# Kernel optimization log

Measured on AMD Instinct MI355X. Metric: run time of the kernel, lower is better.

The kernel has to match this reference:

```python
import jax, jax.numpy as jnp
import numpy as np

N_FFT = 2048
HOP = 512
OUT_CH = N_FFT // 2 + 1  # 1025


def _dft_conv_weights():
    # periodic ('fftbins=True') Hann window, win_length == n_fft so no padding
    n = np.arange(N_FFT)
    window = 0.5 - 0.5 * np.cos(2.0 * np.pi * n / N_FFT)
    k = np.arange(OUT_CH)
    ang = 2.0 * np.pi * np.outer(k, n) / N_FFT  # (OUT_CH, N_FFT)
    w_real = (np.cos(ang) * window[None, :]).astype(np.float32)
    w_imag = (-np.sin(ang) * window[None, :]).astype(np.float32)
    return jnp.asarray(w_real), jnp.asarray(w_imag)


def setup_inputs() -> dict:
    key = jax.random.key(0)
    x = jax.random.normal(key, (32, 2, 160000), dtype=jnp.float32)
    W_real, W_imag = _dft_conv_weights()
    return {"x": x, "W_real": W_real, "W_imag": W_imag}


def reference(x, W_real, W_imag):
    # x: (B, C, L). center=True -> reflect pad by n_fft//2 on both sides.
    pad = N_FFT // 2
    x_pad = jnp.pad(x, ((0, 0), (0, 0), (pad, pad)), mode="reflect")
    L = x_pad.shape[-1]
    num_frames = (L - N_FFT) // HOP + 1  # 313
    # frame indices: (T, N_FFT)
    idx = jnp.arange(num_frames)[:, None] * HOP + jnp.arange(N_FFT)[None, :]
    frames = x_pad[..., idx]  # (B, C, T, N_FFT)
    # windowed DFT as matmul (equivalent to the Conv1d with stride=hop)
    real = jnp.einsum("bctn,kn->bctk", frames, W_real)
    imag = jnp.einsum("bctn,kn->bctk", frames, W_imag)
    return real, imag
```

## Files before the change

kernel.cpp:

```cpp
#include <hip/hip_runtime.h>

#define B_     32
#define C_     2
#define L_     160000
#define HOP    512
#define PAD    1024
#define LPAD   162048
#define T_     313
#define BC     64
#define M_     20032
#define KCH    1025
#define OUT_HALF 20532800UL
#define PL     81024
#define KD     1024
#define NKT    32
#define MTP    160
#define NWG    1280
#define LIMW   8336

typedef __attribute__((ext_vector_type(8))) short short8;
typedef __attribute__((ext_vector_type(4))) float f32x4;

static __device__ __forceinline__ short f2bf(float f) {
  union { float f; unsigned u; } v; v.f = f;
  unsigned u = v.u;
  unsigned r = (u + 0x7fffu + ((u >> 16) & 1u)) >> 16;
  return (short)r;
}

__global__ void prep_planes(const float* __restrict__ x,
                            short* __restrict__ pl0, short* __restrict__ pl1) {
  int v = blockIdx.x * 256 + threadIdx.x;
  int bc = v / 10128;
  int r  = v - bc * 10128;
  int p0 = r * 8;
  const float* src = x + (size_t)bc * L_;
  short8 e, o;
  if (r >= 64 && r <= 10000) {
    int j0 = 16 * r - 1024;
    #pragma unroll
    for (int qq = 0; qq < 4; ++qq) {
      float4 f = *(const float4*)(src + j0 + qq * 4);
      e[qq * 2 + 0] = f2bf(f.x); o[qq * 2 + 0] = f2bf(f.y);
      e[qq * 2 + 1] = f2bf(f.z); o[qq * 2 + 1] = f2bf(f.w);
    }
  } else {
    #pragma unroll
    for (int u = 0; u < 16; ++u) {
      int j = 16 * r + u - 1024;
      j = j < 0 ? -j : j;
      j = j >= L_ ? 2 * L_ - 2 - j : j;
      short b = f2bf(src[j]);
      if (u & 1) o[u >> 1] = b; else e[u >> 1] = b;
    }
  }
  *(short8*)&pl0[(size_t)bc * PL + p0] = e;
  *(short8*)&pl1[(size_t)bc * PL + p0] = o;
}

__global__ void prep_wb(short* __restrict__ wb0, short* __restrict__ wb1) {
  int id = blockIdx.x * 256 + threadIdx.x;
  int s   = id >> 17;
  int row = (id >> 7) & 1023;
  int n8  = (id & 127) * 8;
  int kp  = row >> 1, e = row & 1;
  short8 ov;
  #pragma unroll
  for (int u = 0; u < 8; ++u) {
    int n1 = n8 + u;
    float win = 0.5f - 0.5f * cosf((float)(2 * n1 + s) * 3.0679615757712823e-3f);
    float tw;
    if (e == 0)       tw = cosf((float)((n1 * kp) & 1023) * 6.1359231515425649e-3f);
    else if (kp == 0) tw = (n1 & 1) ? -1.0f : 1.0f;
    else              tw = -sinf((float)((n1 * kp) & 1023) * 6.1359231515425649e-3f);
    ov[u] = f2bf(win * tw);
  }
  short* wb = s ? wb1 : wb0;
  *(short8*)&wb[(size_t)row * KD + n8] = ov;
}

#define GLOAD16(g, l) __builtin_amdgcn_global_load_lds(                        \
    (const __attribute__((address_space(1))) void*)(g),                        \
    (__attribute__((address_space(3))) void*)(l), 16, 0, 0)

__global__ __launch_bounds__(512, 4) void stft_gemm(const short* __restrict__ pl0,
                                                    const short* __restrict__ pl1,
                                                    const short* __restrict__ wb0,
                                                    const short* __restrict__ wb1,
                                                    float* __restrict__ out) {
  __shared__ __align__(16) char lds[66688];
  const int tid  = threadIdx.x;
  const int lane = tid & 63;
  const int wid  = tid >> 6;

  const int id = blockIdx.x;
  const int mt = (id & 7) * 20 + (id >> 6);
  const int nt = (id >> 3) & 7;
  const int M0 = mt * 128, N0 = nt * 128;

  const int sw = wid & 1, wn = (wid >> 1) & 1, wm = wid >> 2;

  const int srow  = tid >> 2;
  const int chunk = ((tid & 3) ^ ((tid >> 3) & 3)) * 8;
  const short *a0S, *a1S, *b0S, *b1S;
  {
    int m = M0 + srow; if (m > M_ - 1) m = M_ - 1;
    int bc = m / T_;
    int t  = m - bc * T_;
    size_t base = (size_t)bc * PL + (size_t)t * 256 + chunk;
    a0S = pl0 + base;
    a1S = pl1 + base;
    size_t bb = (size_t)(N0 + srow) * KD + chunk;
    b0S = wb0 + bb;
    b1S = wb1 + bb;
  }
  const int dst = tid * 16;

  const int fr = lane & 15;
  const int xorb = ((lane >> 4) * 16) ^ ((fr & 6) << 3);
  int aOff[4], bOff[4];
  #pragma unroll
  for (int i = 0; i < 4; ++i)
    aOff[i] = sw * 8192 + (wm * 64 + i * 16 + fr) * 64 + xorb;
  #pragma unroll
  for (int j = 0; j < 4; ++j)
    bOff[j] = 16384 + sw * 8192 + (wn * 64 + j * 16 + fr) * 64 + xorb;

  f32x4 acc[4][4];
  #pragma unroll
  for (int i = 0; i < 4; ++i)
    #pragma unroll
    for (int j = 0; j < 4; ++j) acc[i][j] = (f32x4){0.f, 0.f, 0.f, 0.f};

  GLOAD16(a0S, lds + dst);
  GLOAD16(a1S, lds + 8192 + dst);
  GLOAD16(b0S, lds + 16384 + dst);
  GLOAD16(b1S, lds + 24576 + dst);

  for (int kt = 0; kt < NKT; ++kt) {
    char* bufR = lds + (kt & 1) * 32768;
    char* bufW = lds + ((kt + 1) & 1) * 32768;
    const int kos = (kt + 1) * 32;
    const bool st = (kt < NKT - 1);

    if (st) {
      GLOAD16(a0S + kos, bufW + dst);
      GLOAD16(a1S + kos, bufW + 8192 + dst);
      GLOAD16(b0S + kos, bufW + 16384 + dst);
      GLOAD16(b1S + kos, bufW + 24576 + dst);
      asm volatile("s_waitcnt vmcnt(4)" ::: "memory");
    } else {
      asm volatile("s_waitcnt vmcnt(0)" ::: "memory");
    }
    __builtin_amdgcn_s_barrier();

    short8 af[4], bf[4];
    #pragma unroll
    for (int i = 0; i < 4; ++i) af[i] = *(const short8*)(bufR + aOff[i]);
    #pragma unroll
    for (int j = 0; j < 4; ++j) bf[j] = *(const short8*)(bufR + bOff[j]);
    __builtin_amdgcn_s_setprio(1);
    #pragma unroll
    for (int i = 0; i < 4; ++i)
      #pragma unroll
      for (int j = 0; j < 4; ++j)
        acc[i][j] = __builtin_amdgcn_mfma_f32_16x16x32_bf16(af[i], bf[j],
                                                            acc[i][j], 0, 0, 0);
    __builtin_amdgcn_s_setprio(0);
    __builtin_amdgcn_s_barrier();
  }

  float* L = (float*)lds;
  float* outI = out + OUT_HALF;
  const float PIQ = 3.0679615757712823e-3f;
  const int rgrp = (lane >> 4) << 2;

  __syncthreads();

  #pragma unroll
  for (int pass = 0; pass < 2; ++pass) {
    if (sw == 0) {
      #pragma unroll
      for (int j = 0; j < 4; ++j) {
        int c  = wn * 64 + j * 16 + fr;
        int q  = c >> 1;
        bool odd  = c & 1;
        bool spec = (nt == 0) && (c == 1);
        int widx = (odd ? LIMW : 0) + (pass ? (63 - q) : q);
        #pragma unroll
        for (int i = 0; i < 4; ++i) {
          int row = wm * 64 + i * 16 + rgrp;
          #pragma unroll
          for (int r = 0; r < 4; ++r) {
            float v0 = acc[i][j][r];
            float base = pass == 0 ? v0 : (odd ? -v0 : v0);
            if (spec) base = 0.f;
            L[widx + (row + r) * 65] = base;
            if (spec && pass == 0) {
              int gm = M0 + row + r;
              if (gm < M_) out[(size_t)gm * KCH + 512] = v0;
            }
          }
        }
      }
    }
    __syncthreads();
    if (sw == 1) {
      #pragma unroll
      for (int j = 0; j < 4; ++j) {
        int c  = wn * 64 + j * 16 + fr;
        int q  = c >> 1;
        float ang = (float)(nt * 64 + q) * PIQ;
        float tr = cosf(ang), sn = sinf(ang);
        bool odd  = c & 1;
        bool spec = (nt == 0) && (c == 1);
        float sgn = odd ? -sn : sn;
        int widx = (odd ? LIMW : 0) + (pass ? (63 - q) : q);
        #pragma unroll
        for (int i = 0; i < 4; ++i) {
          int row = wm * 64 + i * 16 + rgrp;
          #pragma unroll
          for (int r = 0; r < 4; ++r) {
            float v1 = acc[i][j][r];
            float p1 = __shfl_xor(v1, 1);
            float u  = tr * v1 + sgn * p1;
            if (!spec) {
              float addv = (pass == 0) ? u : (odd ? u : -u);
              int li = widx + (row + r) * 65;
              L[li] += addv;
            } else if (pass == 0) {
              int gm = M0 + row + r;
              if (gm < M_) outI[(size_t)gm * KCH + 512] = -v1;
            }
          }
        }
      }
    }
    __syncthreads();
    {
      int col0 = pass ? (1024 - nt * 64 - 63) : (nt * 64);
      #pragma unroll
      for (int i2 = 0; i2 < 16; ++i2) {
        int row = wid + i2 * 8;
        int gm  = M0 + row;
        if (gm < M_) {
          size_t rb = (size_t)gm * KCH + col0 + lane;
          out [rb] = L[row * 65 + lane];
          outI[rb] = L[LIMW + row * 65 + lane];
        }
      }
    }
    __syncthreads();
  }
}

extern "C" void kernel_launch(void* const* d_in, const int* in_sizes, int n_in,
                              void* d_out, int out_size, void* d_ws, size_t ws_size,
                              hipStream_t stream) {
  const float* x = (const float*)d_in[0];
  float* out = (float*)d_out;

  short* pl0 = (short*)d_ws;
  short* pl1 = pl0 + (size_t)BC * PL;
  short* wb0 = pl1 + (size_t)BC * PL;
  short* wb1 = wb0 + (size_t)1024 * KD;

  prep_planes<<<2532, 256, 0, stream>>>(x, pl0, pl1);
  prep_wb<<<1024, 256, 0, stream>>>(wb0, wb1);

  stft_gemm<<<NWG, 512, 0, stream>>>(pl0, pl1, wb0, wb1, out);
}
```

Baseline: 147.8 us.

## Load GEMM operands directly from global memory into registers, dropping LDS staging

Replaces the double-buffered global-to-LDS staging of A and B tiles (with barriers) by direct per-lane vector loads from global memory into MFMA fragment registers. The intent is to remove LDS traffic and the two barriers per k-step. In exchange, each wave now fetches its own operands with no sharing inside the workgroup, so global/L2 traffic rises and there is no software prefetch to hide load latency.

```diff
diff --git a/kernel.cpp b/kernel.cpp
--- a/kernel.cpp
+++ b/kernel.cpp
@@ -79,10 +79,6 @@
   *(short8*)&wb[(size_t)row * KD + n8] = ov;
 }
 
-#define GLOAD16(g, l) __builtin_amdgcn_global_load_lds(                        \
-    (const __attribute__((address_space(1))) void*)(g),                        \
-    (__attribute__((address_space(3))) void*)(l), 16, 0, 0)
-
 __global__ __launch_bounds__(512, 4) void stft_gemm(const short* __restrict__ pl0,
                                                     const short* __restrict__ pl1,
                                                     const short* __restrict__ wb0,
@@ -100,65 +96,39 @@
 
   const int sw = wid & 1, wn = (wid >> 1) & 1, wm = wid >> 2;
 
-  const int srow  = tid >> 2;
-  const int chunk = ((tid & 3) ^ ((tid >> 3) & 3)) * 8;
-  const short *a0S, *a1S, *b0S, *b1S;
-  {
-    int m = M0 + srow; if (m > M_ - 1) m = M_ - 1;
+  const int fr = lane & 15;
+  const int kh = lane >> 4;
+  const short* plS = sw ? pl1 : pl0;
+  const short* wbS = sw ? wb1 : wb0;
+  const short* aPtr[4];
+  const short* bPtr[4];
+  #pragma unroll
+  for (int i = 0; i < 4; ++i) {
+    int m = M0 + wm * 64 + i * 16 + fr;
+    if (m > M_ - 1) m = M_ - 1;
     int bc = m / T_;
     int t  = m - bc * T_;
-    size_t base = (size_t)bc * PL + (size_t)t * 256 + chunk;
-    a0S = pl0 + base;
-    a1S = pl1 + base;
-    size_t bb = (size_t)(N0 + srow) * KD + chunk;
-    b0S = wb0 + bb;
-    b1S = wb1 + bb;
-  }
-  const int dst = tid * 16;
-
-  const int fr = lane & 15;
-  const int xorb = ((lane >> 4) * 16) ^ ((fr & 6) << 3);
-  int aOff[4], bOff[4];
+    aPtr[i] = plS + (size_t)bc * PL + (size_t)t * 256 + kh * 8;
+  }
+  #pragma unroll
+  for (int j = 0; j < 4; ++j) {
+    int n = N0 + wn * 64 + j * 16 + fr;
+    bPtr[j] = wbS + (size_t)n * KD + kh * 8;
+  }
+
+  f32x4 acc[4][4];
   #pragma unroll
   for (int i = 0; i < 4; ++i)
-    aOff[i] = sw * 8192 + (wm * 64 + i * 16 + fr) * 64 + xorb;
-  #pragma unroll
-  for (int j = 0; j < 4; ++j)
-    bOff[j] = 16384 + sw * 8192 + (wn * 64 + j * 16 + fr) * 64 + xorb;
-
-  f32x4 acc[4][4];
-  #pragma unroll
-  for (int i = 0; i < 4; ++i)
     #pragma unroll
     for (int j = 0; j < 4; ++j) acc[i][j] = (f32x4){0.f, 0.f, 0.f, 0.f};
 
-  GLOAD16(a0S, lds + dst);
-  GLOAD16(a1S, lds + 8192 + dst);
-  GLOAD16(b0S, lds + 16384 + dst);
-  GLOAD16(b1S, lds + 24576 + dst);
-
   for (int kt = 0; kt < NKT; ++kt) {
-    char* bufR = lds + (kt & 1) * 32768;
-    char* bufW = lds + ((kt + 1) & 1) * 32768;
-    const int kos = (kt + 1) * 32;
-    const bool st = (kt < NKT - 1);
-
-    if (st) {
-      GLOAD16(a0S + kos, bufW + dst);
-      GLOAD16(a1S + kos, bufW + 8192 + dst);
-      GLOAD16(b0S + kos, bufW + 16384 + dst);
-      GLOAD16(b1S + kos, bufW + 24576 + dst);
-      asm volatile("s_waitcnt vmcnt(4)" ::: "memory");
-    } else {
-      asm volatile("s_waitcnt vmcnt(0)" ::: "memory");
-    }
-    __builtin_amdgcn_s_barrier();
-
+    const int ko = kt * 32;
     short8 af[4], bf[4];
     #pragma unroll
-    for (int i = 0; i < 4; ++i) af[i] = *(const short8*)(bufR + aOff[i]);
-    #pragma unroll
-    for (int j = 0; j < 4; ++j) bf[j] = *(const short8*)(bufR + bOff[j]);
+    for (int i = 0; i < 4; ++i) af[i] = *(const short8*)(aPtr[i] + ko);
+    #pragma unroll
+    for (int j = 0; j < 4; ++j) bf[j] = *(const short8*)(bPtr[j] + ko);
     __builtin_amdgcn_s_setprio(1);
     #pragma unroll
     for (int i = 0; i < 4; ++i)
@@ -167,7 +137,6 @@
         acc[i][j] = __builtin_amdgcn_mfma_f32_16x16x32_bf16(af[i], bf[j],
                                                             acc[i][j], 0, 0, 0);
     __builtin_amdgcn_s_setprio(0);
-    __builtin_amdgcn_s_barrier();
   }
 
   float* L = (float*)lds;
```

Measured after the change: 320.1 us. +116.6%, slower.
